# Kernel tuning notes

Hardware: AMD Instinct MI355X
Metric: run time of the kernel (lower is better)

The kernel has to match this reference:

```python
import jax, jax.numpy as jnp
import numpy as np

H = 64
IN_DIM = 32
N = 50000
E = 100000
B = 500


def setup_inputs() -> dict:
    key = jax.random.key(0)
    ks = jax.random.split(key, 16)
    def rn(k, shape, s=0.05):
        return jax.random.normal(k, shape, dtype=jnp.float32) * s
    inp = dict(
        nfeat=rn(ks[0], (N, IN_DIM), 1.0),
        efeat=rn(ks[1], (E, 5), 1.0),
        lin0_w=rn(ks[2], (IN_DIM, H)), lin0_b=jnp.zeros((H,), jnp.float32),
        ew1=rn(ks[3], (5, 128)), eb1=jnp.zeros((128,), jnp.float32),
        ew2=rn(ks[4], (128, H * H)), eb2=jnp.zeros((H * H,), jnp.float32),
        conv_b=jnp.zeros((H,), jnp.float32),
        gru_wih=rn(ks[5], (3 * H, H)), gru_whh=rn(ks[6], (3 * H, H)),
        gru_bih=jnp.zeros((3 * H,), jnp.float32), gru_bhh=jnp.zeros((3 * H,), jnp.float32),
        lstm_wih=rn(ks[7], (4 * H, 2 * H)), lstm_whh=rn(ks[8], (4 * H, H)),
        lstm_bih=jnp.zeros((4 * H,), jnp.float32), lstm_bhh=jnp.zeros((4 * H,), jnp.float32),
        fc1_w=rn(ks[9], (2 * H, H)), fc1_b=jnp.zeros((H,), jnp.float32),
        fc2_w=rn(ks[10], (H, 1)), fc2_b=jnp.zeros((1,), jnp.float32),
        src=jax.random.randint(ks[11], (E,), 0, N),
        dst=jax.random.randint(ks[12], (E,), 0, N),
        graph_id=jnp.arange(N) // (N // B),  # B graphs of equal size, sorted
        num_graphs=B,
    )
    return inp


def reference(nfeat, efeat, lin0_w, lin0_b, ew1, eb1, ew2, eb2, conv_b,
              gru_wih, gru_whh, gru_bih, gru_bhh,
              lstm_wih, lstm_whh, lstm_bih, lstm_bhh,
              fc1_w, fc1_b, fc2_w, fc2_b,
              src, dst, graph_id, num_graphs):
    n_nodes = nfeat.shape[0]
    # lin0 + relu
    h = jax.nn.relu(nfeat @ lin0_w + lin0_b)  # [N, H]
    # edge-conditioned weight matrices (same for all 3 iterations)
    We = (jax.nn.relu(efeat @ ew1 + eb1) @ ew2 + eb2).reshape(-1, H, H)  # [E, H, H]
    deg = jnp.maximum(
        jax.ops.segment_sum(jnp.ones(src.shape[0], jnp.float32), dst, num_segments=n_nodes), 1.0)
    for _ in range(3):
        # NNConv: gather src feats, per-edge matmul, scatter-mean at dst
        msg = jnp.einsum('eh,eho->eo', h[src], We)  # [E, H]
        agg = jax.ops.segment_sum(msg, dst, num_segments=n_nodes) / deg[:, None]
        m = jax.nn.relu(agg + conv_b)
        # GRU step (PyTorch gate order r,z,n)
        gi = m @ gru_wih.T + gru_bih
        gh = h @ gru_whh.T + gru_bhh
        r = jax.nn.sigmoid(gi[:, :H] + gh[:, :H])
        z = jax.nn.sigmoid(gi[:, H:2 * H] + gh[:, H:2 * H])
        n = jnp.tanh(gi[:, 2 * H:] + r * gh[:, 2 * H:])
        h = (1.0 - z) * n + z * h
    feat = h  # [N, H]
    # Set2Set pooling: 3 iters, 1-layer LSTM with input 2H
    q_star = jnp.zeros((num_graphs, 2 * H), jnp.float32)
    hh = jnp.zeros((num_graphs, H), jnp.float32)
    cc = jnp.zeros((num_graphs, H), jnp.float32)
    for _ in range(3):
        gates = q_star @ lstm_wih.T + lstm_bih + hh @ lstm_whh.T + lstm_bhh
        i = jax.nn.sigmoid(gates[:, :H])
        f = jax.nn.sigmoid(gates[:, H:2 * H])
        g = jnp.tanh(gates[:, 2 * H:3 * H])
        o = jax.nn.sigmoid(gates[:, 3 * H:])
        cc = f * cc + i * g
        hh = o * jnp.tanh(cc)
        q = hh  # [B, H]
        e = jnp.sum(feat * q[graph_id], axis=-1)  # [N]
        emax = jax.ops.segment_max(e, graph_id, num_segments=num_graphs)
        alpha = jnp.exp(e - emax[graph_id])
        denom = jax.ops.segment_sum(alpha, graph_id, num_segments=num_graphs)
        alpha = alpha / denom[graph_id]
        readout = jax.ops.segment_sum(alpha[:, None] * feat, graph_id, num_segments=num_graphs)
        q_star = jnp.concatenate([q, readout], axis=-1)  # [B, 2H]
    pred = jax.nn.relu(q_star @ fc1_w + fc1_b) @ fc2_w + fc2_b  # [B, 1]
    return pred.reshape(-1)
```

## Files before the change

### kernel.cpp

```cpp
#include <hip/hip_runtime.h>

#define HD 64
#define NNODE 50000
#define NEDGE 100000
#define NGR 500
#define NPG 100
#define EPAD 100352
#define NCH 66

typedef _Float16 f16;
typedef _Float16 f16x2 __attribute__((ext_vector_type(2)));
typedef _Float16 f16x8 __attribute__((ext_vector_type(8)));
typedef float f32x4 __attribute__((ext_vector_type(4)));

__device__ __forceinline__ float sigmoidf_(float x) { return 1.f / (1.f + __expf(-x)); }

#define G_NODE 12500
#define G_EMLP 3136
#define G_GRU  48
#define G_T1   128
#define G_T2   64
#define G_IDX  392
#define G_ALL (G_NODE + G_EMLP + G_GRU + G_T1 + G_T2 + G_IDX)

__global__ __launch_bounds__(256) void k_prep_all(
    const float* __restrict__ nfeat, const float* __restrict__ lin0_w, const float* __restrict__ lin0_b,
    const float* __restrict__ efeat, const float* __restrict__ ew1, const float* __restrict__ eb1,
    const float* __restrict__ gwih, const float* __restrict__ gwhh,
    const float* __restrict__ lwih, const float* __restrict__ lwhh,
    const int* __restrict__ src, const int* __restrict__ dst,
    float* __restrict__ h, f16* __restrict__ uE,
    f16* __restrict__ gB1, f16* __restrict__ gB2,
    float* __restrict__ lwihT, float* __restrict__ lwhhT,
    int* __restrict__ srcP, int* __restrict__ dstP, int* __restrict__ cnt) {
    int bb = blockIdx.x;
    int t = threadIdx.x;
    if (bb < G_NODE) {
        int idx = bb * 256 + t;
        int n = idx >> 6, o = idx & 63;
        if (n >= NNODE) return;
        const float* nf = nfeat + n * 32;
        float acc = lin0_b[o];
#pragma unroll
        for (int i = 0; i < 32; i++) acc += nf[i] * lin0_w[i * 64 + o];
        h[idx] = fmaxf(acc, 0.f);
        return;
    }
    bb -= G_NODE;
    if (bb < G_EMLP) {
        __shared__ float sw[5 * 128];
        __shared__ float sb[128];
        for (int idx = t; idx < 640; idx += 256) sw[idx] = ew1[idx];
        if (t < 128) sb[t] = eb1[t];
        __syncthreads();
        int idx = bb * 256 + t;
        int e = idx >> 3, grp = idx & 7;
        bool valid = e < NEDGE;
        float ef[5];
#pragma unroll
        for (int i = 0; i < 5; i++) ef[i] = valid ? efeat[e * 5 + i] : 0.f;
        f16x8 v0, v1;
#pragma unroll
        for (int s = 0; s < 8; s++) {
            int k = grp * 16 + s;
            float acc = sb[k];
#pragma unroll
            for (int i = 0; i < 5; i++) acc += ef[i] * sw[i * 128 + k];
            v0[s] = valid ? (f16)fmaxf(acc, 0.f) : (f16)0.f;
        }
#pragma unroll
        for (int s = 0; s < 8; s++) {
            int k = grp * 16 + 8 + s;
            float acc = sb[k];
#pragma unroll
            for (int i = 0; i < 5; i++) acc += ef[i] * sw[i * 128 + k];
            v1[s] = valid ? (f16)fmaxf(acc, 0.f) : (f16)0.f;
        }
        *(f16x8*)(uE + (size_t)e * 128 + grp * 16) = v0;
        *(f16x8*)(uE + (size_t)e * 128 + grp * 16 + 8) = v1;
        return;
    }
    bb -= G_EMLP;
    if (bb < G_GRU) {
        int idx = bb * 256 + t;
        int cp = idx >> 6, k = idx & 63;
        int w = cp / 48, rem = cp % 48;
        int tg = rem >> 4, cc = rem & 15;
        int orow = tg * 64 + w * 16 + cc;
        gB1[idx] = (f16)gwih[orow * 64 + k];
        gB2[idx] = (f16)gwhh[orow * 64 + k];
        return;
    }
    bb -= G_GRU;
    if (bb < G_T1) {
        int idx = bb * 256 + t;
        int r = idx >> 7, c = idx & 127;
        lwihT[c * 256 + r] = lwih[idx];
        return;
    }
    bb -= G_T1;
    if (bb < G_T2) {
        int idx = bb * 256 + t;
        int r = idx >> 6, c = idx & 63;
        lwhhT[c * 256 + r] = lwhh[idx];
        return;
    }
    bb -= G_T2;
    {
        int e = bb * 256 + t;
        if (e >= EPAD) return;
        if (e < NEDGE) {
            int d = dst[e];
            srcP[e] = src[e];
            dstP[e] = d;
            atomicAdd(&cnt[d], 1);
        } else {
            srcP[e] = 0;
            dstP[e] = -1;
        }
    }
}

__global__ __launch_bounds__(256) void k_pack_b(const float* __restrict__ ew2,
                                                const float* __restrict__ eb2,
                                                f16* __restrict__ w2hp) {
    __shared__ float s[8192];
    int c = blockIdx.x, t = threadIdx.x;
    for (int i = t; i < 8192; i += 256) {
        int kg = c * 128 + (i >> 6);
        float v = 0.f;
        if (kg < 8192) v = ew2[(size_t)c * 8192 + i];
        else if (kg < 8256) v = eb2[(kg - 8192) * 64 + (i & 63)];
        s[i] = v;
    }
    __syncthreads();
    f16* outp = w2hp + (size_t)c * 8192 + t * 32;
#pragma unroll
    for (int ff = 0; ff < 4; ff++) {
        int F = t * 4 + ff;
        int l = F & 63, ks = (F >> 6) & 3, ch2 = F >> 8;
        int sl = (F >> 8) & 3;
        int jj = (F >> 6) & 3;
        (void)ks; (void)ch2;
        f16x8 v;
#pragma unroll
        for (int q = 0; q < 8; q++)
            v[q] = (f16)s[(sl * 32 + ((l >> 4) << 3) + q) * 64 + jj * 16 + (l & 15)];
        *(f16x8*)(outp + ff * 8) = v;
    }
}

__global__ void k_deg_inv(const int* __restrict__ cnt, float* __restrict__ dinv) {
    int n = blockIdx.x * 256 + threadIdx.x;
    if (n < NNODE) dinv[n] = 1.f / (float)max(cnt[n], 1);
}

#define ISSUE(BUF, CN)                                                                  \
    {                                                                                   \
        const f16x8* bp = gBp + (size_t)(CN) * 1024;                                    \
        _Pragma("unroll") for (int s = 0; s < 8; s++)                                   \
            BUF[s] = bp[(s >> 1) * 256 + (s & 1) * 64];                                 \
    }
#define COMP(BUF, CL)                                                                   \
    {                                                                                   \
        _Pragma("unroll") for (int sl = 0; sl < 4; sl++)                                \
            _Pragma("unroll") for (int i = 0; i < 8; i++) {                             \
                f16x8 av = xf[i][sl & 1] * uc[i][2 * (CL) + (sl >> 1)];                 \
                acc[i][0] = __builtin_amdgcn_mfma_f32_16x16x32_f16(av, BUF[sl * 2], acc[i][0], 0, 0, 0);     \
                acc[i][1] = __builtin_amdgcn_mfma_f32_16x16x32_f16(av, BUF[sl * 2 + 1], acc[i][1], 0, 0, 0); \
            }                                                                           \
    }

__global__ __launch_bounds__(64, 1) void k_msg_fused(
    const float* __restrict__ h, const f16* __restrict__ uE, const f16* __restrict__ w2hp,
    const int* __restrict__ srcP, const int* __restrict__ dstP, float* __restrict__ agg) {
    int l = threadIdx.x;
    int wid = blockIdx.x;
    int eb = (wid >> 1) * 128;
    int ch = wid & 1;
    int lr = l & 15, lg = l >> 4;
    f16x8 xf[8][2];
#pragma unroll
    for (int i = 0; i < 8; i++) {
        const float* xb = h + (size_t)srcP[eb + i * 16 + lr] * 64;
#pragma unroll
        for (int p = 0; p < 2; p++) {
            float4 v0 = *(const float4*)(xb + p * 32 + lg * 8);
            float4 v1 = *(const float4*)(xb + p * 32 + lg * 8 + 4);
            f16x8 xv;
            xv[0] = (f16)v0.x; xv[1] = (f16)v0.y; xv[2] = (f16)v0.z; xv[3] = (f16)v0.w;
            xv[4] = (f16)v1.x; xv[5] = (f16)v1.y; xv[6] = (f16)v1.z; xv[7] = (f16)v1.w;
            xf[i][p] = xv;
        }
    }
    const f16x8* gBp = (const f16x8*)w2hp + ch * 128 + l;
    f32x4 acc[8][2];
#pragma unroll
    for (int i = 0; i < 8; i++) {
        acc[i][0] = (f32x4){0.f, 0.f, 0.f, 0.f};
        acc[i][1] = (f32x4){0.f, 0.f, 0.f, 0.f};
    }
    f16x8 b0[8], b1[8], b2[8], b3[8], bz[4];
    ISSUE(b0, 0)
    ISSUE(b1, 1)
    ISSUE(b2, 2)
#pragma unroll
    for (int s = 0; s < 4; s++)
        bz[s] = gBp[(size_t)64 * 1024 + (s >> 1) * 256 + (s & 1) * 64];
    f16x8 uc[8], un[8];
#pragma unroll
    for (int i = 0; i < 8; i++)
        uc[i] = *((const f16x8*)(uE + (size_t)(eb + i * 16 + lr) * 128));
#pragma unroll 1
    for (int it = 0; it < 15; it++) {
        int c = it * 4;
#pragma unroll
        for (int i = 0; i < 8; i++)
            un[i] = *((const f16x8*)(uE + (size_t)(eb + i * 16 + lr) * 128) + (it + 1));
        ISSUE(b3, c + 3) COMP(b0, 0)
        ISSUE(b0, c + 4) COMP(b1, 1)
        ISSUE(b1, c + 5) COMP(b2, 2)
        ISSUE(b2, c + 6) COMP(b3, 3)
#pragma unroll
        for (int i = 0; i < 8; i++) uc[i] = un[i];
    }
    ISSUE(b3, 63)
    COMP(b0, 0) COMP(b1, 1) COMP(b2, 2) COMP(b3, 3)
#pragma unroll
    for (int sl = 0; sl < 2; sl++)
#pragma unroll
        for (int i = 0; i < 8; i++) {
            acc[i][0] = __builtin_amdgcn_mfma_f32_16x16x32_f16(xf[i][sl], bz[sl * 2], acc[i][0], 0, 0, 0);
            acc[i][1] = __builtin_amdgcn_mfma_f32_16x16x32_f16(xf[i][sl], bz[sl * 2 + 1], acc[i][1], 0, 0, 0);
        }
#pragma unroll
    for (int i = 0; i < 8; i++) {
        int rb = eb + i * 16 + lg * 4;
        int4 d4 = *(const int4*)(dstP + rb);
#pragma unroll
        for (int r = 0; r < 4; r++) {
            int d = (r == 0) ? d4.x : (r == 1) ? d4.y : (r == 2) ? d4.z : d4.w;
            if (d >= 0) {
                float* ap = agg + (size_t)d * 64 + ch * 32 + lr;
                atomicAdd(ap, acc[i][0][r]);
                atomicAdd(ap + 16, acc[i][1][r]);
            }
        }
    }
}

#define GWP 72
__global__ __launch_bounds__(256) void k_gru2(float* __restrict__ agg,
                                              const float* __restrict__ dinv,
                                              const float* __restrict__ convb,
                                              const f16* __restrict__ B1g,
                                              const f16* __restrict__ B2g,
                                              const float* __restrict__ bih,
                                              const float* __restrict__ bhh,
                                              float* __restrict__ h) {
    __shared__ f16 sM[64 * GWP];
    __shared__ f16 sH[64 * GWP];
    int t = threadIdx.x;
    int nb = blockIdx.x * 64;
    int w = t >> 6, l = t & 63, lr = l & 15, lg = l >> 4;
    f16x8 b1[2][3], b2[2][3];
#pragma unroll
    for (int kk = 0; kk < 2; kk++)
#pragma unroll
        for (int j = 0; j < 3; j++) {
            size_t off = (size_t)(w * 48 + j * 16 + lr) * 64 + kk * 32 + lg * 8;
            b1[kk][j] = *(const f16x8*)(B1g + off);
            b2[kk][j] = *(const f16x8*)(B2g + off);
        }
#pragma unroll
    for (int it = 0; it < 16; it++) {
        int idx = t + 256 * it;
        int node = idx >> 6, k = idx & 63;
        int gn = nb + node;
        float mv = 0.f, hv = 0.f;
        if (gn < NNODE) {
            size_t off = (size_t)gn * 64 + k;
            mv = fmaxf(agg[off] * dinv[gn] + convb[k], 0.f);
            hv = h[off];
            agg[off] = 0.f;
        }
        sM[node * GWP + k] = (f16)mv;
        sH[node * GWP + k] = (f16)hv;
    }
    __syncthreads();
    f32x4 aih[4][3], ahh[4][3];
#pragma unroll
    for (int i = 0; i < 4; i++)
#pragma unroll
        for (int j = 0; j < 3; j++) {
            aih[i][j] = (f32x4){0.f, 0.f, 0.f, 0.f};
            ahh[i][j] = (f32x4){0.f, 0.f, 0.f, 0.f};
        }
#pragma unroll
    for (int kk = 0; kk < 2; kk++) {
        f16x8 am[4], ah[4];
#pragma unroll
        for (int i = 0; i < 4; i++) {
            am[i] = *(const f16x8*)(sM + (i * 16 + lr) * GWP + kk * 32 + lg * 8);
            ah[i] = *(const f16x8*)(sH + (i * 16 + lr) * GWP + kk * 32 + lg * 8);
        }
#pragma unroll
        for (int i = 0; i < 4; i++)
#pragma unroll
            for (int j = 0; j < 3; j++) {
                aih[i][j] = __builtin_amdgcn_mfma_f32_16x16x32_f16(am[i], b1[kk][j], aih[i][j], 0, 0, 0);
                ahh[i][j] = __builtin_amdgcn_mfma_f32_16x16x32_f16(ah[i], b2[kk][j], ahh[i][j], 0, 0, 0);
            }
    }
    float bi0 = bih[0 * 64 + w * 16 + lr], bh0 = bhh[0 * 64 + w * 16 + lr];
    float bi1 = bih[1 * 64 + w * 16 + lr], bh1 = bhh[1 * 64 + w * 16 + lr];
    float bi2 = bih[2 * 64 + w * 16 + lr], bh2 = bhh[2 * 64 + w * 16 + lr];
#pragma unroll
    for (int i = 0; i < 4; i++)
#pragma unroll
        for (int r = 0; r < 4; r++) {
            int node = i * 16 + lg * 4 + r;
            int gn = nb + node;
            if (gn >= NNODE) continue;
            float rg = sigmoidf_(aih[i][0][r] + bi0 + ahh[i][0][r] + bh0);
            float z = sigmoidf_(aih[i][1][r] + bi1 + ahh[i][1][r] + bh1);
            float nn = tanhf(aih[i][2][r] + bi2 + rg * (ahh[i][2][r] + bh2));
            size_t off = (size_t)gn * 64 + w * 16 + lr;
            float hold = h[off];
            h[off] = (1.f - z) * nn + z * hold;
        }
}

#define FP 68
__global__ __launch_bounds__(256) void k_s2s(const float* __restrict__ feat,
                                             const float* __restrict__ wihT,
                                             const float* __restrict__ whhT,
                                             const float* __restrict__ lbih,
                                             const float* __restrict__ lbhh,
                                             const float* __restrict__ fc1w,
                                             const float* __restrict__ fc1b,
                                             const float* __restrict__ fc2w,
                                             const float* __restrict__ fc2b,
                                             float* __restrict__ out) {
    __shared__ float sf[NPG * FP];
    __shared__ float sq[128];
    __shared__ float sh[64], scc[64];
    __shared__ float sg[256];
    __shared__ float se[NPG];
    __shared__ float red[2];
    int g = blockIdx.x, t = threadIdx.x;
    const float* fb = feat + (size_t)g * NPG * 64;
    for (int idx = t; idx < NPG * 64; idx += 256)
        sf[(idx >> 6) * FP + (idx & 63)] = fb[idx];
    if (t < 128) sq[t] = 0.f;
    if (t >= 128 && t < 192) { sh[t - 128] = 0.f; scc[t - 128] = 0.f; }
    __syncthreads();
    for (int it = 0; it < 3; it++) {
        float gate = lbih[t] + lbhh[t];
#pragma unroll 8
        for (int i = 0; i < 128; i++) gate += sq[i] * wihT[i * 256 + t];
#pragma unroll 8
        for (int i = 0; i < 64; i++) gate += sh[i] * whhT[i * 256 + t];
        sg[t] = gate;
        __syncthreads();
        if (t < 64) {
            float ig = sigmoidf_(sg[t]);
            float fg = sigmoidf_(sg[64 + t]);
            float gg = tanhf(sg[128 + t]);
            float og = sigmoidf_(sg[192 + t]);
            float c = fg * scc[t] + ig * gg;
            scc[t] = c;
            float hv = og * tanhf(c);
            sh[t] = hv;
            sq[t] = hv;
        }
        __syncthreads();
        if (t < NPG) {
            float e = 0.f;
#pragma unroll 8
            for (int o = 0; o < 64; o++) e += sf[t * FP + o] * sh[o];
            se[t] = e;
        }
        __syncthreads();
        if (t < 64) {
            float m = -1e30f;
            for (int i2 = t; i2 < NPG; i2 += 64) m = fmaxf(m, se[i2]);
            for (int d = 32; d; d >>= 1) m = fmaxf(m, __shfl_down(m, d));
            if (t == 0) red[0] = m;
        }
        __syncthreads();
        float emax = red[0];
        if (t < NPG) se[t] = __expf(se[t] - emax);
        __syncthreads();
        if (t < 64) {
            float s = 0.f;
            for (int i2 = t; i2 < NPG; i2 += 64) s += se[i2];
            for (int d = 32; d; d >>= 1) s += __shfl_down(s, d);
            if (t == 0) red[1] = s;
        }
        __syncthreads();
        if (t < 64) {
            float dnv = 1.f / red[1];
            float r = 0.f;
#pragma unroll 4
            for (int n = 0; n < NPG; n++) r += se[n] * sf[n * FP + t];
            sq[64 + t] = r * dnv;
        }
        __syncthreads();
    }
    if (t < 64) {
        float hsum = fc1b[t];
#pragma unroll 8
        for (int i = 0; i < 128; i++) hsum += sq[i] * fc1w[i * 64 + t];
        float p = fmaxf(hsum, 0.f) * fc2w[t];
        for (int d = 32; d; d >>= 1) p += __shfl_down(p, d);
        if (t == 0) out[g] = p + fc2b[0];
    }
}

extern "C" void kernel_launch(void* const* d_in, const int* in_sizes, int n_in,
                              void* d_out, int out_size, void* d_ws, size_t ws_size,
                              hipStream_t stream) {
    const float* nfeat = (const float*)d_in[0];
    const float* efeat = (const float*)d_in[1];
    const float* lin0_w = (const float*)d_in[2];
    const float* lin0_b = (const float*)d_in[3];
    const float* ew1 = (const float*)d_in[4];
    const float* eb1 = (const float*)d_in[5];
    const float* ew2 = (const float*)d_in[6];
    const float* eb2 = (const float*)d_in[7];
    const float* convb = (const float*)d_in[8];
    const float* gwih = (const float*)d_in[9];
    const float* gwhh = (const float*)d_in[10];
    const float* gbih = (const float*)d_in[11];
    const float* gbhh = (const float*)d_in[12];
    const float* lwih = (const float*)d_in[13];
    const float* lwhh = (const float*)d_in[14];
    const float* lbih = (const float*)d_in[15];
    const float* lbhh = (const float*)d_in[16];
    const float* fc1w = (const float*)d_in[17];
    const float* fc1b = (const float*)d_in[18];
    const float* fc2w = (const float*)d_in[19];
    const float* fc2b = (const float*)d_in[20];
    const int* src = (const int*)d_in[21];
    const int* dst = (const int*)d_in[22];
    float* out = (float*)d_out;

    char* p = (char*)d_ws;
    auto alloc = [&](size_t bytes) {
        char* q = p;
        p += (bytes + 255) & ~(size_t)255;
        return q;
    };
    f16* uE = (f16*)alloc((size_t)EPAD * 128 * 2 + 256);
    f16* w2hp = (f16*)alloc((size_t)NCH * 8192 * 2);
    float* h = (float*)alloc((size_t)NNODE * 64 * 4);
    float* agg = (float*)alloc((size_t)NNODE * 64 * 4);
    int* cnt = (int*)alloc((size_t)NNODE * 4);
    float* dinv = (float*)alloc((size_t)NNODE * 4);
    float* lwihT = (float*)alloc((size_t)128 * 256 * 4);
    float* lwhhT = (float*)alloc((size_t)64 * 256 * 4);
    f16* gB1 = (f16*)alloc((size_t)12288 * 2);
    f16* gB2 = (f16*)alloc((size_t)12288 * 2);
    int* srcP = (int*)alloc((size_t)EPAD * 4);
    int* dstP = (int*)alloc((size_t)EPAD * 4);
    if ((size_t)(p - (char*)d_ws) > ws_size) return;

    hipMemsetAsync(cnt, 0, (size_t)NNODE * 4, stream);
    hipMemsetAsync(agg, 0, (size_t)NNODE * 64 * 4, stream);

    k_prep_all<<<G_ALL, 256, 0, stream>>>(nfeat, lin0_w, lin0_b, efeat, ew1, eb1,
                                          gwih, gwhh, lwih, lwhh, src, dst,
                                          h, uE, gB1, gB2, lwihT, lwhhT, srcP, dstP, cnt);
    k_pack_b<<<NCH, 256, 0, stream>>>(ew2, eb2, w2hp);
    k_deg_inv<<<(NNODE + 255) / 256, 256, 0, stream>>>(cnt, dinv);

    for (int it = 0; it < 3; it++) {
        k_msg_fused<<<(EPAD / 128) * 2, 64, 0, stream>>>(h, uE, w2hp, srcP, dstP, agg);
        k_gru2<<<(NNODE + 63) / 64, 256, 0, stream>>>(agg, dinv, convb, gB1, gB2, gbih, gbhh, h);
    }
    k_s2s<<<NGR, 256, 0, stream>>>(h, lwihT, lwhhT, lbih, lbhh, fc1w, fc1b, fc2w, fc2b, out);
}
```

Baseline: 566.0 us.

## Replace atomic scatter with CSR gather and restructure edge message kernel tiling

The per-edge message kernel now writes each edge's message to a buffer instead of atomically adding into per-node aggregates. A counting-sort CSR (scan kernels plus placement of edge ids) lets the GRU kernel sum incoming messages per destination by gathering, which also removes the agg memset and reset. The edge MLP output is stored in a channel-major packed f16x2 layout, and the message kernel switches to 64 edges per wave, full 64 output columns and a double-buffered weight pipeline. This trades atomics for an extra 25MB message buffer round trip, irregular gathers through eid, and several more small setup launches.

Result: slower. 639.3 us (+12.9%).

```diff
diff --git a/kernel.cpp b/kernel.cpp
--- a/kernel.cpp
+++ b/kernel.cpp
@@ -16,7 +16,7 @@
 __device__ __forceinline__ float sigmoidf_(float x) { return 1.f / (1.f + __expf(-x)); }
 
 #define G_NODE 12500
-#define G_EMLP 3136
+#define G_EMLP 392
 #define G_GRU  48
 #define G_T1   128
 #define G_T2   64
@@ -29,10 +29,10 @@
     const float* __restrict__ gwih, const float* __restrict__ gwhh,
     const float* __restrict__ lwih, const float* __restrict__ lwhh,
     const int* __restrict__ src, const int* __restrict__ dst,
-    float* __restrict__ h, f16* __restrict__ uE,
+    float* __restrict__ h, f16x2* __restrict__ uP,
     f16* __restrict__ gB1, f16* __restrict__ gB2,
     float* __restrict__ lwihT, float* __restrict__ lwhhT,
-    int* __restrict__ srcP, int* __restrict__ dstP, int* __restrict__ cnt) {
+    int* __restrict__ srcP, int* __restrict__ cnt) {
     int bb = blockIdx.x;
     int t = threadIdx.x;
     if (bb < G_NODE) {
@@ -53,31 +53,27 @@
         for (int idx = t; idx < 640; idx += 256) sw[idx] = ew1[idx];
         if (t < 128) sb[t] = eb1[t];
         __syncthreads();
-        int idx = bb * 256 + t;
-        int e = idx >> 3, grp = idx & 7;
+        int e = bb * 256 + t;
         bool valid = e < NEDGE;
         float ef[5];
 #pragma unroll
         for (int i = 0; i < 5; i++) ef[i] = valid ? efeat[e * 5 + i] : 0.f;
-        f16x8 v0, v1;
-#pragma unroll
-        for (int s = 0; s < 8; s++) {
-            int k = grp * 16 + s;
-            float acc = sb[k];
-#pragma unroll
-            for (int i = 0; i < 5; i++) acc += ef[i] * sw[i * 128 + k];
-            v0[s] = valid ? (f16)fmaxf(acc, 0.f) : (f16)0.f;
-        }
-#pragma unroll
-        for (int s = 0; s < 8; s++) {
-            int k = grp * 16 + 8 + s;
-            float acc = sb[k];
-#pragma unroll
-            for (int i = 0; i < 5; i++) acc += ef[i] * sw[i * 128 + k];
-            v1[s] = valid ? (f16)fmaxf(acc, 0.f) : (f16)0.f;
-        }
-        *(f16x8*)(uE + (size_t)e * 128 + grp * 16) = v0;
-        *(f16x8*)(uE + (size_t)e * 128 + grp * 16 + 8) = v1;
+#pragma unroll 2
+        for (int c = 0; c < 64; c++) {
+            float v[2];
+#pragma unroll
+            for (int s = 0; s < 2; s++) {
+                int k = 2 * c + s;
+                float acc = sb[k];
+#pragma unroll
+                for (int i = 0; i < 5; i++) acc += ef[i] * sw[i * 128 + k];
+                v[s] = valid ? fmaxf(acc, 0.f) : 0.f;
+            }
+            f16x2 pv;
+            pv[0] = (f16)v[0];
+            pv[1] = (f16)v[1];
+            uP[(size_t)c * EPAD + e] = pv;
+        }
         return;
     }
     bb -= G_EMLP;
@@ -110,13 +106,10 @@
         int e = bb * 256 + t;
         if (e >= EPAD) return;
         if (e < NEDGE) {
-            int d = dst[e];
             srcP[e] = src[e];
-            dstP[e] = d;
-            atomicAdd(&cnt[d], 1);
+            atomicAdd(&cnt[dst[e]], 1);
         } else {
             srcP[e] = 0;
-            dstP[e] = -1;
         }
     }
 }
@@ -138,10 +131,9 @@
 #pragma unroll
     for (int ff = 0; ff < 4; ff++) {
         int F = t * 4 + ff;
-        int l = F & 63, ks = (F >> 6) & 3, ch2 = F >> 8;
+        int l = F & 63;
+        int jj = (F >> 6) & 3;
         int sl = (F >> 8) & 3;
-        int jj = (F >> 6) & 3;
-        (void)ks; (void)ch2;
         f16x8 v;
 #pragma unroll
         for (int q = 0; q < 8; q++)
@@ -150,38 +142,84 @@
     }
 }
 
-__global__ void k_deg_inv(const int* __restrict__ cnt, float* __restrict__ dinv) {
-    int n = blockIdx.x * 256 + threadIdx.x;
-    if (n < NNODE) dinv[n] = 1.f / (float)max(cnt[n], 1);
-}
-
-#define ISSUE(BUF, CN)                                                                  \
+__global__ __launch_bounds__(256) void k_scanA(const int* __restrict__ cnt,
+                                               int* __restrict__ excl, int* __restrict__ bpart) {
+    __shared__ int s[256];
+    int t = threadIdx.x;
+    int g = blockIdx.x * 256 + t;
+    int v = (g < NNODE) ? cnt[g] : 0;
+    s[t] = v;
+    __syncthreads();
+#pragma unroll
+    for (int d = 1; d < 256; d <<= 1) {
+        int x = (t >= d) ? s[t - d] : 0;
+        __syncthreads();
+        s[t] += x;
+        __syncthreads();
+    }
+    if (g < NNODE) excl[g] = s[t] - v;
+    if (t == 255) bpart[blockIdx.x] = s[255];
+}
+__global__ __launch_bounds__(256) void k_scanB(int* __restrict__ bpart, int nb) {
+    __shared__ int s[256];
+    int t = threadIdx.x;
+    int v = (t < nb) ? bpart[t] : 0;
+    s[t] = v;
+    __syncthreads();
+#pragma unroll
+    for (int d = 1; d < 256; d <<= 1) {
+        int x = (t >= d) ? s[t - d] : 0;
+        __syncthreads();
+        s[t] += x;
+        __syncthreads();
+    }
+    if (t < nb) bpart[t] = s[t] - v;
+}
+__global__ __launch_bounds__(256) void k_scanC(const int* __restrict__ excl,
+                                               const int* __restrict__ bpart,
+                                               const int* __restrict__ cnt,
+                                               int* __restrict__ rowptr, int* __restrict__ woff,
+                                               float* __restrict__ dinv) {
+    int g = blockIdx.x * 256 + threadIdx.x;
+    if (g == 0) rowptr[NNODE] = NEDGE;
+    if (g >= NNODE) return;
+    int r = excl[g] + bpart[blockIdx.x];
+    rowptr[g] = r;
+    woff[g] = r;
+    dinv[g] = 1.f / (float)max(cnt[g], 1);
+}
+__global__ __launch_bounds__(256) void k_place(const int* __restrict__ dst,
+                                               int* __restrict__ woff, int* __restrict__ eid) {
+    int e = blockIdx.x * 256 + threadIdx.x;
+    if (e >= NEDGE) return;
+    int slot = atomicAdd(&woff[dst[e]], 1);
+    eid[slot] = e;
+}
+
+#define ISSUEB(BUF, HC)                                                                 \
     {                                                                                   \
-        const f16x8* bp = gBp + (size_t)(CN) * 1024;                                    \
-        _Pragma("unroll") for (int s = 0; s < 8; s++)                                   \
-            BUF[s] = bp[(s >> 1) * 256 + (s & 1) * 64];                                 \
-    }
-#define COMP(BUF, CL)                                                                   \
+        const f16x8* bp = gB + (size_t)(HC) * 512 + l;                                  \
+        _Pragma("unroll") for (int s = 0; s < 8; s++) BUF[s] = bp[s * 64];              \
+    }
+#define COMPH(BUF, BIT)                                                                 \
     {                                                                                   \
-        _Pragma("unroll") for (int sl = 0; sl < 4; sl++)                                \
-            _Pragma("unroll") for (int i = 0; i < 8; i++) {                             \
-                f16x8 av = xf[i][sl & 1] * uc[i][2 * (CL) + (sl >> 1)];                 \
-                acc[i][0] = __builtin_amdgcn_mfma_f32_16x16x32_f16(av, BUF[sl * 2], acc[i][0], 0, 0, 0);     \
-                acc[i][1] = __builtin_amdgcn_mfma_f32_16x16x32_f16(av, BUF[sl * 2 + 1], acc[i][1], 0, 0, 0); \
+        _Pragma("unroll") for (int ks = 0; ks < 2; ks++)                                \
+            _Pragma("unroll") for (int i = 0; i < 4; i++) {                             \
+                f16x8 av = xf[i][ks] * uc[i][BIT];                                      \
+                _Pragma("unroll") for (int j = 0; j < 4; j++)                           \
+                    acc[i][j] = __builtin_amdgcn_mfma_f32_16x16x32_f16(av, BUF[ks * 4 + j], acc[i][j], 0, 0, 0); \
             }                                                                           \
     }
 
-__global__ __launch_bounds__(64, 1) void k_msg_fused(
-    const float* __restrict__ h, const f16* __restrict__ uE, const f16* __restrict__ w2hp,
-    const int* __restrict__ srcP, const int* __restrict__ dstP, float* __restrict__ agg) {
+__global__ __launch_bounds__(64) void k_msg(
+    const float* __restrict__ h, const f16x2* __restrict__ uP, const f16* __restrict__ w2hp,
+    const int* __restrict__ srcP, float* __restrict__ msgbuf) {
     int l = threadIdx.x;
-    int wid = blockIdx.x;
-    int eb = (wid >> 1) * 128;
-    int ch = wid & 1;
+    int eb = blockIdx.x * 64;
     int lr = l & 15, lg = l >> 4;
-    f16x8 xf[8][2];
-#pragma unroll
-    for (int i = 0; i < 8; i++) {
+    f16x8 xf[4][2];
+#pragma unroll
+    for (int i = 0; i < 4; i++) {
         const float* xb = h + (size_t)srcP[eb + i * 16 + lr] * 64;
 #pragma unroll
         for (int p = 0; p < 2; p++) {
@@ -193,64 +231,51 @@
             xf[i][p] = xv;
         }
     }
-    const f16x8* gBp = (const f16x8*)w2hp + ch * 128 + l;
-    f32x4 acc[8][2];
-#pragma unroll
-    for (int i = 0; i < 8; i++) {
-        acc[i][0] = (f32x4){0.f, 0.f, 0.f, 0.f};
-        acc[i][1] = (f32x4){0.f, 0.f, 0.f, 0.f};
-    }
-    f16x8 b0[8], b1[8], b2[8], b3[8], bz[4];
-    ISSUE(b0, 0)
-    ISSUE(b1, 1)
-    ISSUE(b2, 2)
-#pragma unroll
-    for (int s = 0; s < 4; s++)
-        bz[s] = gBp[(size_t)64 * 1024 + (s >> 1) * 256 + (s & 1) * 64];
-    f16x8 uc[8], un[8];
-#pragma unroll
-    for (int i = 0; i < 8; i++)
-        uc[i] = *((const f16x8*)(uE + (size_t)(eb + i * 16 + lr) * 128));
+    const f16x8* gB = (const f16x8*)w2hp;
+    f32x4 acc[4][4];
+#pragma unroll
+    for (int i = 0; i < 4; i++)
+#pragma unroll
+        for (int j = 0; j < 4; j++) acc[i][j] = (f32x4){0.f, 0.f, 0.f, 0.f};
+    f16x8 bA[8], bB[8];
+    f16x2 uc[4], un[4];
+    ISSUEB(bA, 0)
+#pragma unroll
+    for (int i = 0; i < 4; i++) uc[i] = uP[eb + i * 16 + lr];
 #pragma unroll 1
-    for (int it = 0; it < 15; it++) {
-        int c = it * 4;
-#pragma unroll
-        for (int i = 0; i < 8; i++)
-            un[i] = *((const f16x8*)(uE + (size_t)(eb + i * 16 + lr) * 128) + (it + 1));
-        ISSUE(b3, c + 3) COMP(b0, 0)
-        ISSUE(b0, c + 4) COMP(b1, 1)
-        ISSUE(b1, c + 5) COMP(b2, 2)
-        ISSUE(b2, c + 6) COMP(b3, 3)
-#pragma unroll
-        for (int i = 0; i < 8; i++) uc[i] = un[i];
-    }
-    ISSUE(b3, 63)
-    COMP(b0, 0) COMP(b1, 1) COMP(b2, 2) COMP(b3, 3)
-#pragma unroll
-    for (int sl = 0; sl < 2; sl++)
-#pragma unroll
-        for (int i = 0; i < 8; i++) {
-            acc[i][0] = __builtin_amdgcn_mfma_f32_16x16x32_f16(xf[i][sl], bz[sl * 2], acc[i][0], 0, 0, 0);
-            acc[i][1] = __builtin_amdgcn_mfma_f32_16x16x32_f16(xf[i][sl], bz[sl * 2 + 1], acc[i][1], 0, 0, 0);
-        }
-#pragma unroll
-    for (int i = 0; i < 8; i++) {
-        int rb = eb + i * 16 + lg * 4;
-        int4 d4 = *(const int4*)(dstP + rb);
+    for (int c = 0; c < 64; c++) {
+        ISSUEB(bB, 2 * c + 1)
+        int cn = (c < 63) ? c + 1 : 63;
+#pragma unroll
+        for (int i = 0; i < 4; i++) un[i] = uP[(size_t)cn * EPAD + eb + i * 16 + lr];
+        COMPH(bA, 0)
+        ISSUEB(bA, 2 * c + 2)
+        COMPH(bB, 1)
+#pragma unroll
+        for (int i = 0; i < 4; i++) uc[i] = un[i];
+    }
+#pragma unroll
+    for (int ks = 0; ks < 2; ks++)
+#pragma unroll
+        for (int i = 0; i < 4; i++)
+#pragma unroll
+            for (int j = 0; j < 4; j++)
+                acc[i][j] = __builtin_amdgcn_mfma_f32_16x16x32_f16(xf[i][ks], bA[ks * 4 + j], acc[i][j], 0, 0, 0);
+#pragma unroll
+    for (int i = 0; i < 4; i++) {
 #pragma unroll
         for (int r = 0; r < 4; r++) {
-            int d = (r == 0) ? d4.x : (r == 1) ? d4.y : (r == 2) ? d4.z : d4.w;
-            if (d >= 0) {
-                float* ap = agg + (size_t)d * 64 + ch * 32 + lr;
-                atomicAdd(ap, acc[i][0][r]);
-                atomicAdd(ap + 16, acc[i][1][r]);
-            }
+            float* mp = msgbuf + (size_t)(eb + i * 16 + lg * 4 + r) * 64 + lr;
+#pragma unroll
+            for (int j = 0; j < 4; j++) mp[j * 16] = acc[i][j][r];
         }
     }
 }
 
 #define GWP 72
-__global__ __launch_bounds__(256) void k_gru2(float* __restrict__ agg,
+__global__ __launch_bounds__(256) void k_gru3(const float* __restrict__ msgbuf,
+                                              const int* __restrict__ rowptr,
+                                              const int* __restrict__ eid,
                                               const float* __restrict__ dinv,
                                               const float* __restrict__ convb,
                                               const f16* __restrict__ B1g,
@@ -260,8 +285,10 @@
                                               float* __restrict__ h) {
     __shared__ f16 sM[64 * GWP];
     __shared__ f16 sH[64 * GWP];
+    __shared__ int srp[65];
     int t = threadIdx.x;
     int nb = blockIdx.x * 64;
+    if (t < 65) srp[t] = rowptr[min(nb + t, NNODE)];
     int w = t >> 6, l = t & 63, lr = l & 15, lg = l >> 4;
     f16x8 b1[2][3], b2[2][3];
 #pragma unroll
@@ -272,6 +299,7 @@
             b1[kk][j] = *(const f16x8*)(B1g + off);
             b2[kk][j] = *(const f16x8*)(B2g + off);
         }
+    __syncthreads();
 #pragma unroll
     for (int it = 0; it < 16; it++) {
         int idx = t + 256 * it;
@@ -279,10 +307,11 @@
         int gn = nb + node;
         float mv = 0.f, hv = 0.f;
         if (gn < NNODE) {
-            size_t off = (size_t)gn * 64 + k;
-            mv = fmaxf(agg[off] * dinv[gn] + convb[k], 0.f);
-            hv = h[off];
-            agg[off] = 0.f;
+            float m_raw = 0.f;
+            int s0 = srp[node], s1 = srp[node + 1];
+            for (int s = s0; s < s1; s++) m_raw += msgbuf[(size_t)eid[s] * 64 + k];
+            mv = fmaxf(m_raw * dinv[gn] + convb[k], 0.f);
+            hv = h[(size_t)gn * 64 + k];
         }
         sM[node * GWP + k] = (f16)mv;
         sH[node * GWP + k] = (f16)hv;
@@ -452,32 +481,40 @@
         p += (bytes + 255) & ~(size_t)255;
         return q;
     };
-    f16* uE = (f16*)alloc((size_t)EPAD * 128 * 2 + 256);
+    f16x2* uP = (f16x2*)alloc((size_t)64 * EPAD * 4);
     f16* w2hp = (f16*)alloc((size_t)NCH * 8192 * 2);
     float* h = (float*)alloc((size_t)NNODE * 64 * 4);
-    float* agg = (float*)alloc((size_t)NNODE * 64 * 4);
+    float* msgbuf = (float*)alloc((size_t)EPAD * 64 * 4);
     int* cnt = (int*)alloc((size_t)NNODE * 4);
     float* dinv = (float*)alloc((size_t)NNODE * 4);
+    int* rowptr = (int*)alloc((size_t)(NNODE + 1) * 4);
+    int* woff = (int*)alloc((size_t)NNODE * 4);
+    int* excl = (int*)alloc((size_t)NNODE * 4);
+    int* bpart = (int*)alloc((size_t)256 * 4);
+    int* eid = (int*)alloc((size_t)NEDGE * 4);
     float* lwihT = (float*)alloc((size_t)128 * 256 * 4);
     float* lwhhT = (float*)alloc((size_t)64 * 256 * 4);
     f16* gB1 = (f16*)alloc((size_t)12288 * 2);
     f16* gB2 = (f16*)alloc((size_t)12288 * 2);
     int* srcP = (int*)alloc((size_t)EPAD * 4);
-    int* dstP = (int*)alloc((size_t)EPAD * 4);
     if ((size_t)(p - (char*)d_ws) > ws_size) return;
 
     hipMemsetAsync(cnt, 0, (size_t)NNODE * 4, stream);
-    hipMemsetAsync(agg, 0, (size_t)NNODE * 64 * 4, stream);
 
     k_prep_all<<<G_ALL, 256, 0, stream>>>(nfeat, lin0_w, lin0_b, efeat, ew1, eb1,
                                           gwih, gwhh, lwih, lwhh, src, dst,
-                                          h, uE, gB1, gB2, lwihT, lwhhT, srcP, dstP, cnt);
+                                          h, uP, gB1, gB2, lwihT, lwhhT, srcP, cnt);
     k_pack_b<<<NCH, 256, 0, stream>>>(ew2, eb2, w2hp);
-    k_deg_inv<<<(NNODE + 255) / 256, 256, 0, stream>>>(cnt, dinv);
+    int nsb = (NNODE + 255) / 256;
+    k_scanA<<<nsb, 256, 0, stream>>>(cnt, excl, bpart);
+    k_scanB<<<1, 256, 0, stream>>>(bpart, nsb);
+    k_scanC<<<nsb, 256, 0, stream>>>(excl, bpart, cnt, rowptr, woff, dinv);
+    k_place<<<(NEDGE + 255) / 256, 256, 0, stream>>>(dst, woff, eid);
 
     for (int it = 0; it < 3; it++) {
-        k_msg_fused<<<(EPAD / 128) * 2, 64, 0, stream>>>(h, uE, w2hp, srcP, dstP, agg);
-        k_gru2<<<(NNODE + 63) / 64, 256, 0, stream>>>(agg, dinv, convb, gB1, gB2, gbih, gbhh, h);
+        k_msg<<<EPAD / 64, 64, 0, stream>>>(h, uP, w2hp, srcP, msgbuf);
+        k_gru3<<<(NNODE + 63) / 64, 256, 0, stream>>>(msgbuf, rowptr, eid, dinv, convb,
+                                                      gB1, gB2, gbih, gbhh, h);
     }
     k_s2s<<<NGR, 256, 0, stream>>>(h, lwihT, lwhhT, lbih, lbhh, fc1w, fc1b, fc2w, fc2b, out);
 }
```
